# Performance work log

Hardware: AMD Instinct MI355X
Metric: run time of the kernel (lower is better)

The kernel has to match this reference:

```python
import jax, jax.numpy as jnp
import numpy as np

B, D_IN, H, A, L, HEADS, C = 1024, 512, 768, 5001, 4, 2, 2
N_DATA = 56000.0
NEG = -1e30


def _gru_step(x, h, Wih, Whh, bih, bhh):
    # torch nn.GRU gate order: r, z, n
    gi = x @ Wih + bih            # [B, 3H]
    gh = h @ Whh + bhh            # [B, 3H]
    i_r, i_z, i_n = jnp.split(gi, 3, axis=-1)
    h_r, h_z, h_n = jnp.split(gh, 3, axis=-1)
    r = jax.nn.sigmoid(i_r + h_r)
    z = jax.nn.sigmoid(i_z + h_z)
    n = jnp.tanh(i_n + r * h_n)
    return (1.0 - z) * n + z * h


def _atom_selector(cls, mask, Wih, Whh, bih, bhh, hW, hb, ae_w, key):
    # cls: [B, H]; mask: [B, A] int32 (mutable copy); dropout in eval mode (identity)
    h = jnp.zeros_like(cls)
    cur_in = cls
    ae_const = jax.lax.stop_gradient(ae_w)
    probs = []
    max_index = None
    rows = jnp.arange(B)
    for j in range(L):
        h = _gru_step(cur_in, h, Wih, Whh, bih, bhh)
        logits = h @ hW + hb                      # [B, A]
        if j == 0:
            col0 = jnp.where(mask.sum(axis=-1) == 0, 1, mask[:, 0])
            mask = mask.at[:, 0].set(col0)
        else:
            mask = jnp.where((max_index == 0)[:, None], 0, mask)
            mask = mask.at[:, 0].set(1)
        masked = jnp.where(mask > 0, logits, NEG)
        u = jax.random.uniform(jax.random.fold_in(key, j), (B, A), minval=1e-9, maxval=1.0)
        g = -jnp.log(-jnp.log(u))
        y_soft = jax.nn.softmax(masked + g, axis=-1)  # tau = 1
        ind = jnp.argmax(y_soft, axis=-1)             # [B]
        y_hard = jax.nn.one_hot(ind, A, dtype=y_soft.dtype)
        prob = y_hard + y_soft - jax.lax.stop_gradient(y_soft)  # straight-through
        mask = mask.at[rows, ind].set(0)              # scatter-zero chosen atoms
        probs.append(prob)
        max_index = ind
        cur_in = cls + prob @ ae_const                # atom embedding feedback
    return jnp.stack(probs, axis=1)                   # [B, L, A]


def reference(x, x_mask, W1, b1, W2, b2, W3, b3, gru_Wih, gru_Whh, gru_bih, gru_bhh,
              head_W, head_b, ae_w, ce_Wmu, ce_bmu, ce_Wcov, ce_bcov, alpha):
    # linear_base MLP
    h = jax.nn.relu(x @ W1 + b1)
    h = jax.nn.relu(h @ W2 + b2)
    h = h @ W3 + b3                                   # cls embedding [B, H]
    key = jax.random.key(42)
    atom_probs, cps = [], []
    for i in range(HEADS):
        ap = _atom_selector(h, x_mask, gru_Wih[i], gru_Whh[i], gru_bih[i], gru_bhh[i],
                            head_W[i], head_b[i], ae_w, jax.random.fold_in(key, i))
        atom_probs.append(ap)
        # consequent estimator stand-in: mu [B,C], coverage [B]
        pooled = ap.mean(axis=1)                      # [B, A]
        mu = jax.nn.sigmoid(pooled @ ce_Wmu + ce_bmu)
        coverage = jax.nn.sigmoid(pooled @ ce_Wcov + ce_bcov)
        n = coverage * N_DATA
        sf = (alpha[0] / n)[:, None]                  # [B, 1] -> broadcast to [B, C]
        cp = (mu + sf) / (1.0 + 2.0 * sf)
        cps.append(cp)
    mat_cp = jnp.stack(cps, axis=1)                   # [B, HEADS, C]
    out = jnp.log(mat_cp.mean(axis=1))                # [B, C]
    return out, jnp.stack(atom_probs, axis=1), mat_cp


def setup_inputs() -> dict:
    key = jax.random.key(0)
    ks = jax.random.split(key, 16)
    s = 0.02
    nrm = lambda k, sh: jax.random.normal(k, sh, dtype=jnp.float32) * s
    return {
        'x': jax.random.normal(ks[0], (B, D_IN), dtype=jnp.float32),
        'x_mask': jax.random.randint(ks[1], (B, A), 0, 2, dtype=jnp.int32),
        'W1': nrm(ks[2], (D_IN, H)), 'b1': jnp.zeros((H,), jnp.float32),
        'W2': nrm(ks[3], (H, H)), 'b2': jnp.zeros((H,), jnp.float32),
        'W3': nrm(ks[4], (H, H)), 'b3': jnp.zeros((H,), jnp.float32),
        'gru_Wih': nrm(ks[5], (HEADS, H, 3 * H)), 'gru_Whh': nrm(ks[6], (HEADS, H, 3 * H)),
        'gru_bih': jnp.zeros((HEADS, 3 * H), jnp.float32), 'gru_bhh': jnp.zeros((HEADS, 3 * H), jnp.float32),
        'head_W': nrm(ks[7], (HEADS, H, A)), 'head_b': jnp.zeros((HEADS, A), jnp.float32),
        'ae_w': nrm(ks[8], (A, H)),
        'ce_Wmu': nrm(ks[9], (A, C)), 'ce_bmu': jnp.zeros((C,), jnp.float32),
        'ce_Wcov': nrm(ks[10], (A,)), 'ce_bcov': jnp.zeros((), jnp.float32),
        'alpha': jnp.ones((1,), jnp.float32),
    }
```

## Files before the change

kernel.cpp:

```cpp
#include <hip/hip_runtime.h>
#include <hip/hip_bf16.h>
#include <stdint.h>
#include <stddef.h>

#define B_DIM   1024
#define DIN     512
#define H_DIM   768
#define A_DIM   5001
#define NHEADS  2
#define NSTEPS  4
#define C_DIM   2
#define NEG_VAL -1e30f
#define BH      (B_DIM * H_DIM)

typedef unsigned short u16;
typedef __attribute__((ext_vector_type(8))) short v8s;
typedef __attribute__((ext_vector_type(4))) float v4f;

typedef const __attribute__((address_space(1))) uint32_t* gas_ptr;
typedef __attribute__((address_space(3))) uint32_t* las_ptr;

__device__ __forceinline__ void load_lds16(const void* g, void* l) {
  __builtin_amdgcn_global_load_lds((gas_ptr)g, (las_ptr)l, 16, 0, 0);
}

__host__ __device__ inline uint32_t rotl32(uint32_t x, int d) {
  return (x << d) | (x >> (32 - d));
}

__host__ __device__ inline void threefry2x32(uint32_t k0, uint32_t k1,
                                             uint32_t x0, uint32_t x1,
                                             uint32_t& o0, uint32_t& o1) {
  uint32_t ks2 = k0 ^ k1 ^ 0x1BD11BDAu;
  x0 += k0; x1 += k1;
#define TFR(d) { x0 += x1; x1 = rotl32(x1, (d)); x1 ^= x0; }
  TFR(13) TFR(15) TFR(26) TFR(6)  x0 += k1;  x1 += ks2 + 1u;
  TFR(17) TFR(29) TFR(16) TFR(24) x0 += ks2; x1 += k0 + 2u;
  TFR(13) TFR(15) TFR(26) TFR(6)  x0 += k0;  x1 += k1 + 3u;
  TFR(17) TFR(29) TFR(16) TFR(24) x0 += k1;  x1 += ks2 + 4u;
  TFR(13) TFR(15) TFR(26) TFR(6)  x0 += ks2; x1 += k0 + 5u;
#undef TFR
  o0 = x0; o1 = x1;
}

__device__ inline float gumbel_noise(uint32_t k0, uint32_t k1, uint32_t idx) {
  uint32_t o0, o1;
  threefry2x32(k0, k1, 0u, idx, o0, o1);
  uint32_t bits = o0 ^ o1;
  float f = __uint_as_float(0x3f800000u | (bits >> 9)) - 1.0f;
  float u = fmaxf(1e-9f, f * (1.0f - 1e-9f) + 1e-9f);
  return -logf(-logf(u));
}

__device__ inline float sigmoidf_(float x) { return 0.5f * tanhf(0.5f * x) + 0.5f; }

__device__ inline void split_bf16(float x, u16& hi, u16& lo) {
  __hip_bfloat16 h = __float2bfloat16(x);
  float hf = __bfloat162float(h);
  __hip_bfloat16 l = __float2bfloat16(x - hf);
  hi = *(const u16*)&h;
  lo = *(const u16*)&l;
}

__global__ __launch_bounds__(256) void gemm_splitk(
    const float* __restrict__ A, const float* __restrict__ B,
    float* __restrict__ part, int M, int N, int K, int kchunk) {
  __shared__ float As[16][65];
  __shared__ float Bs[16][64];
  int tid = threadIdx.x;
  int bm = blockIdx.y * 64, bn = blockIdx.x * 64;
  const int s = blockIdx.z;
  const int kb = s * kchunk;
  const int ke = (kb + kchunk < K) ? (kb + kchunk) : K;
  int tx = tid & 15, ty = tid >> 4;
  float acc[4][4] = {};
  for (int k0 = kb; k0 < ke; k0 += 16) {
#pragma unroll
    for (int r = 0; r < 4; ++r) {
      int m = (tid >> 4) + r * 16;
      int k = tid & 15;
      As[k][m] = A[(size_t)(bm + m) * K + k0 + k];
    }
#pragma unroll
    for (int r = 0; r < 4; ++r) {
      int n = tid & 63;
      int k = (tid >> 6) + r * 4;
      int gn = bn + n;
      Bs[k][n] = (gn < N) ? B[(size_t)(k0 + k) * N + gn] : 0.0f;
    }
    __syncthreads();
#pragma unroll
    for (int kk = 0; kk < 16; ++kk) {
      float a[4], bb[4];
#pragma unroll
      for (int i = 0; i < 4; ++i) a[i] = As[kk][ty * 4 + i];
#pragma unroll
      for (int jj = 0; jj < 4; ++jj) bb[jj] = Bs[kk][tx * 4 + jj];
#pragma unroll
      for (int i = 0; i < 4; ++i)
#pragma unroll
        for (int jj = 0; jj < 4; ++jj) acc[i][jj] = fmaf(a[i], bb[jj], acc[i][jj]);
    }
    __syncthreads();
  }
  float* po = part + (size_t)s * M * N;
#pragma unroll
  for (int i = 0; i < 4; ++i) {
    int m = bm + ty * 4 + i;
#pragma unroll
    for (int jj = 0; jj < 4; ++jj) {
      int n = bn + tx * 4 + jj;
      if (n < N) po[(size_t)m * N + n] = acc[i][jj];
    }
  }
}

__global__ __launch_bounds__(256) void reduce_bias_act(
    const float* __restrict__ part, const float* __restrict__ bias,
    float* __restrict__ C, int M, int N, int S, int act) {
  int idx = blockIdx.x * blockDim.x + threadIdx.x;
  if (idx >= M * N) return;
  int n = idx % N;
  float v = 0.0f;
  for (int s = 0; s < S; ++s) v += part[(size_t)s * M * N + idx];
  v += bias[n];
  if (act == 1) v = fmaxf(v, 0.0f);
  C[idx] = v;
}

__global__ __launch_bounds__(256) void transpose_split(
    const float* __restrict__ W, u16* __restrict__ hi, u16* __restrict__ lo,
    int K, int N, size_t inStride, size_t outStride) {
  const int e = blockIdx.z;
  const float* Win = W + (size_t)e * inStride;
  u16* ho = hi + (size_t)e * outStride;
  u16* loo = lo + (size_t)e * outStride;
  __shared__ float tile[32][33];
  const int k0 = blockIdx.y * 32, n0 = blockIdx.x * 32;
  const int tx = threadIdx.x & 31, ty = threadIdx.x >> 5;
#pragma unroll
  for (int r = ty; r < 32; r += 8) {
    int n = n0 + tx;
    tile[r][tx] = (n < N) ? Win[(size_t)(k0 + r) * N + n] : 0.0f;
  }
  __syncthreads();
#pragma unroll
  for (int r = ty; r < 32; r += 8) {
    int n = n0 + r, k = k0 + tx;
    if (n < N) {
      u16 h, l;
      split_bf16(tile[tx][r], h, l);
      ho[(size_t)n * K + k] = h;
      loo[(size_t)n * K + k] = l;
    }
  }
}

struct GemmS {
  const u16* Ah[4]; const u16* Al[4];
  const u16* Bh[4]; const u16* Bl[4];
  const float* bias[4]; float* C[4];
};

__global__ __launch_bounds__(256, 2) void gemm_mfma(
    GemmS gs, int K, int N, int Nclamp, long long ldc, int nbx, int nby) {
  const int e = blockIdx.y;
  const int nwg = nbx * nby;
  const int chunk = nwg >> 3;
  const int orig = blockIdx.x;
  const int lid = (orig & 7) * chunk + (orig >> 3);
  const int by = lid % nby;
  const int bx = lid / nby;
  const int bm = by * 128, bn = bx * 128;

  __shared__ __align__(16) u16 lds[4][128 * 32];

  const int tid = threadIdx.x;
  const int wv = tid >> 6, ln = tid & 63;
  const int wr = wv >> 1, wc = wv & 1;
  const int lk = ln >> 4;
  const int lm = ln & 15;
  const int fswz = (lm >> 1) & 3;

  const int lrow = ln >> 2;
  const int slot = (ln & 3) ^ ((lrow >> 1) & 3);
  const u16* tsrc = (wv == 0) ? gs.Ah[e] : (wv == 1) ? gs.Al[e]
                  : (wv == 2) ? gs.Bh[e] : gs.Bl[e];
  const int isB = (wv >= 2);
  const int rowbase = isB ? bn : bm;

  const float* bias = gs.bias[e];
  float* C = gs.C[e];

  v4f acc[4][4];
#pragma unroll
  for (int i = 0; i < 4; ++i)
#pragma unroll
    for (int j = 0; j < 4; ++j) acc[i][j] = (v4f){0.f, 0.f, 0.f, 0.f};

  for (int k0 = 0; k0 < K; k0 += 32) {
#pragma unroll
    for (int i = 0; i < 8; ++i) {
      int gr = rowbase + i * 16 + lrow;
      if (isB && gr >= Nclamp) gr = Nclamp - 1;
      const u16* gp = tsrc + (size_t)gr * K + k0 + slot * 8;
      load_lds16(gp, (void*)&lds[wv][i * 512]);
    }
    __syncthreads();

    v8s ah[4], al[4], bh[4], bl[4];
#pragma unroll
    for (int mi = 0; mi < 4; ++mi) {
      const int r = wr * 64 + mi * 16 + lm;
      const int off = r * 32 + ((lk ^ fswz) * 8);
      ah[mi] = *(const v8s*)&lds[0][off];
      al[mi] = *(const v8s*)&lds[1][off];
    }
#pragma unroll
    for (int ni = 0; ni < 4; ++ni) {
      const int r = wc * 64 + ni * 16 + lm;
      const int off = r * 32 + ((lk ^ fswz) * 8);
      bh[ni] = *(const v8s*)&lds[2][off];
      bl[ni] = *(const v8s*)&lds[3][off];
    }
#pragma unroll
    for (int mi = 0; mi < 4; ++mi)
#pragma unroll
      for (int ni = 0; ni < 4; ++ni)
        acc[mi][ni] = __builtin_amdgcn_mfma_f32_16x16x32_bf16(ah[mi], bh[ni], acc[mi][ni], 0, 0, 0);
#pragma unroll
    for (int mi = 0; mi < 4; ++mi)
#pragma unroll
      for (int ni = 0; ni < 4; ++ni)
        acc[mi][ni] = __builtin_amdgcn_mfma_f32_16x16x32_bf16(ah[mi], bl[ni], acc[mi][ni], 0, 0, 0);
#pragma unroll
    for (int mi = 0; mi < 4; ++mi)
#pragma unroll
      for (int ni = 0; ni < 4; ++ni)
        acc[mi][ni] = __builtin_amdgcn_mfma_f32_16x16x32_bf16(al[mi], bh[ni], acc[mi][ni], 0, 0, 0);

    __syncthreads();
  }

#pragma unroll
  for (int mi = 0; mi < 4; ++mi) {
    const int m = bm + wr * 64 + mi * 16 + lk * 4;
#pragma unroll
    for (int ni = 0; ni < 4; ++ni) {
      const int n = bn + wc * 64 + ni * 16 + lm;
      if (n < N) {
        const float bv = bias[n];
        float* cp = C + (size_t)m * ldc + n;
#pragma unroll
        for (int r = 0; r < 4; ++r)
          cp[(size_t)r * ldc] = acc[mi][ni][r] + bv;
      }
    }
  }
}

__global__ __launch_bounds__(256) void init_state_kernel(
    const float* __restrict__ cls,
    u16* __restrict__ cur_hi, u16* __restrict__ cur_lo) {
  int idx = blockIdx.x * blockDim.x + threadIdx.x;
  if (idx >= 2 * BH) return;
  int rem = idx % BH;
  u16 h, l;
  split_bf16(cls[rem], h, l);
  cur_hi[idx] = h; cur_lo[idx] = l;
}

__global__ __launch_bounds__(256) void gru_combine_first(
    const float* __restrict__ gi2, const float* __restrict__ gbhh, float* __restrict__ h2,
    u16* __restrict__ h_hi, u16* __restrict__ h_lo) {
  int idx = blockIdx.x * blockDim.x + threadIdx.x;
  if (idx >= 2 * BH) return;
  int e = idx / BH, rem = idx % BH;
  int b = rem / H_DIM, c = rem - b * H_DIM;
  const float* gib = gi2 + ((size_t)e * B_DIM + b) * 3 * H_DIM;
  const float* bb = gbhh + (size_t)e * 3 * H_DIM;
  float ir = gib[c], iz = gib[H_DIM + c], inn = gib[2 * H_DIM + c];
  float hr = bb[c], hz = bb[H_DIM + c], hn = bb[2 * H_DIM + c];
  float r = sigmoidf_(ir + hr);
  float z = sigmoidf_(iz + hz);
  float n = tanhf(inn + r * hn);
  float hv = (1.0f - z) * n + z * 0.0f;
  h2[idx] = hv;
  u16 h, l;
  split_bf16(hv, h, l);
  h_hi[idx] = h; h_lo[idx] = l;
}

__global__ __launch_bounds__(256) void gru_combine_kernel(
    const float* __restrict__ gi2, const float* __restrict__ gh2, float* __restrict__ h2,
    u16* __restrict__ h_hi, u16* __restrict__ h_lo) {
  int idx = blockIdx.x * blockDim.x + threadIdx.x;
  if (idx >= 2 * BH) return;
  int e = idx / BH, rem = idx % BH;
  int b = rem / H_DIM, c = rem - b * H_DIM;
  const float* gib = gi2 + ((size_t)e * B_DIM + b) * 3 * H_DIM;
  const float* ghb = gh2 + ((size_t)e * B_DIM + b) * 3 * H_DIM;
  float ir = gib[c], iz = gib[H_DIM + c], inn = gib[2 * H_DIM + c];
  float hr = ghb[c], hz = ghb[H_DIM + c], hn = ghb[2 * H_DIM + c];
  float r = sigmoidf_(ir + hr);
  float z = sigmoidf_(iz + hz);
  float n = tanhf(inn + r * hn);
  float hv = (1.0f - z) * n + z * h2[idx];
  h2[idx] = hv;
  u16 h, l;
  split_bf16(hv, h, l);
  h_hi[idx] = h; h_lo[idx] = l;
}

__global__ __launch_bounds__(256) void curin_kernel(
    const float* __restrict__ cls, const float* __restrict__ ae_w,
    const int* __restrict__ indb, int j,
    u16* __restrict__ cur_hi, u16* __restrict__ cur_lo) {
  int idx = blockIdx.x * blockDim.x + threadIdx.x;
  if (idx >= 2 * BH) return;
  int e = idx / BH, rem = idx % BH;
  int b = rem / H_DIM, c = rem - b * H_DIM;
  int ind = indb[(e * NSTEPS + j) * B_DIM + b];
  float v = cls[rem] + ae_w[(size_t)ind * H_DIM + c];
  u16 h, l;
  split_bf16(v, h, l);
  cur_hi[idx] = h; cur_lo[idx] = l;
}

#define STH 256
#define PER_TH 20

__global__ __launch_bounds__(STH) void sample_kernel(
    float* __restrict__ probs, const int* __restrict__ x_mask,
    int* __restrict__ indb, int j, uint4 keys) {
  int b = blockIdx.x;
  int e = blockIdx.y;
  int t = threadIdx.x;
  uint32_t k0 = (e == 0) ? keys.x : keys.z;
  uint32_t k1 = (e == 0) ? keys.y : keys.w;
  __shared__ float rv[STH];
  __shared__ int ri[STH];
  __shared__ int s_ind;

  float* prow = probs + (((size_t)b * NHEADS + e) * NSTEPS + j) * A_DIM;
  const int* mrow = x_mask + (size_t)b * A_DIM;

  int prev[3];
  bool dead = false;
  for (int tt = 0; tt < j; ++tt) {
    prev[tt] = indb[(e * NSTEPS + tt) * B_DIM + b];
    if (prev[tt] == 0) dead = true;
  }

  bool rowany = true;
  if (j == 0) {
    int any = 0;
    for (int a = t; a < A_DIM; a += STH) any |= mrow[a];
    ri[t] = any; __syncthreads();
    for (int s = STH / 2; s > 0; s >>= 1) {
      if (t < s) ri[t] |= ri[t + s];
      __syncthreads();
    }
    rowany = (ri[0] != 0);
    __syncthreads();
  }

  float v[PER_TH];
  float lmax = -3.0e38f;
#pragma unroll
  for (int s = 0; s < PER_TH; ++s) {
    int a = t + s * STH;
    float val = -3.0e38f;
    if (a < A_DIM) {
      int m;
      if (j == 0) {
        m = (a == 0) ? (rowany ? mrow[0] : 1) : mrow[a];
      } else if (a == 0) {
        m = 1;
      } else if (dead) {
        m = 0;
      } else {
        m = mrow[a];
        if (m) {
          for (int tt = 0; tt < j; ++tt)
            if (prev[tt] == a) { m = 0; break; }
        }
      }
      if (m > 0)
        val = prow[a] + gumbel_noise(k0, k1, (uint32_t)(b * A_DIM + a));
    }
    v[s] = val;
    lmax = fmaxf(lmax, val);
  }

  rv[t] = lmax; __syncthreads();
  for (int s = STH / 2; s > 0; s >>= 1) {
    if (t < s) rv[t] = fmaxf(rv[t], rv[t + s]);
    __syncthreads();
  }
  float m = rv[0]; __syncthreads();

  float lsum = 0.0f;
#pragma unroll
  for (int s = 0; s < PER_TH; ++s) {
    int a = t + s * STH;
    float ev = (a < A_DIM && v[s] > -1.0e37f) ? expf(v[s] - m) : 0.0f;
    v[s] = ev; lsum += ev;
  }
  rv[t] = lsum; __syncthreads();
  for (int s = STH / 2; s > 0; s >>= 1) {
    if (t < s) rv[t] += rv[t + s];
    __syncthreads();
  }
  float ssum = rv[0]; __syncthreads();

  float besty = -1.0f; int besti = A_DIM;
#pragma unroll
  for (int s = 0; s < PER_TH; ++s) {
    int a = t + s * STH;
    if (a < A_DIM) {
      float y = v[s] / ssum;
      if (y > besty) { besty = y; besti = a; }
    }
  }
  rv[t] = besty; ri[t] = besti; __syncthreads();
  for (int s = STH / 2; s > 0; s >>= 1) {
    if (t < s) {
      float y2 = rv[t + s]; int i2 = ri[t + s];
      if (y2 > rv[t] || (y2 == rv[t] && i2 < ri[t])) { rv[t] = y2; ri[t] = i2; }
    }
    __syncthreads();
  }
  if (t == 0) { s_ind = ri[0]; indb[(e * NSTEPS + j) * B_DIM + b] = ri[0]; }
  __syncthreads();
  int ind = s_ind;

  for (int a = t; a < A_DIM; a += STH) prow[a] = (a == ind) ? 1.0f : 0.0f;
}

__global__ __launch_bounds__(256) void head_final_kernel(
    const int* __restrict__ indb, const float* __restrict__ Wmu,
    const float* __restrict__ bmu, const float* __restrict__ Wcov,
    const float* __restrict__ bcov, const float* __restrict__ alpha,
    float* __restrict__ matcp) {
  int idx = blockIdx.x * blockDim.x + threadIdx.x;
  if (idx >= NHEADS * B_DIM) return;
  int e = idx / B_DIM, b = idx - e * B_DIM;
  float a0 = 0.0f, a1 = 0.0f, ac = 0.0f;
  for (int j = 0; j < NSTEPS; ++j) {
    int ind = indb[(e * NSTEPS + j) * B_DIM + b];
    a0 += 0.25f * Wmu[(size_t)ind * C_DIM + 0];
    a1 += 0.25f * Wmu[(size_t)ind * C_DIM + 1];
    ac += 0.25f * Wcov[ind];
  }
  float mu0 = sigmoidf_(a0 + bmu[0]);
  float mu1 = sigmoidf_(a1 + bmu[1]);
  float cov = sigmoidf_(ac + bcov[0]);
  float n = cov * 56000.0f;
  float sf = alpha[0] / n;
  float denom = 1.0f + 2.0f * sf;
  matcp[((size_t)b * NHEADS + e) * C_DIM + 0] = (mu0 + sf) / denom;
  matcp[((size_t)b * NHEADS + e) * C_DIM + 1] = (mu1 + sf) / denom;
}

__global__ __launch_bounds__(256) void final_out_kernel(
    const float* __restrict__ matcp, float* __restrict__ out) {
  int idx = blockIdx.x * blockDim.x + threadIdx.x;
  if (idx >= B_DIM * C_DIM) return;
  int b = idx / C_DIM, c = idx - b * C_DIM;
  float s = matcp[((size_t)b * NHEADS + 0) * C_DIM + c] +
            matcp[((size_t)b * NHEADS + 1) * C_DIM + c];
  out[idx] = logf(s * 0.5f);
}

extern "C" void kernel_launch(void* const* d_in, const int* in_sizes, int n_in,
                              void* d_out, int out_size, void* d_ws, size_t ws_size,
                              hipStream_t stream) {
  const float* x     = (const float*)d_in[0];
  const int*   xmask = (const int*)d_in[1];
  const float* W1 = (const float*)d_in[2];  const float* b1 = (const float*)d_in[3];
  const float* W2 = (const float*)d_in[4];  const float* b2 = (const float*)d_in[5];
  const float* W3 = (const float*)d_in[6];  const float* b3 = (const float*)d_in[7];
  const float* gWih = (const float*)d_in[8];  const float* gWhh = (const float*)d_in[9];
  const float* gbih = (const float*)d_in[10]; const float* gbhh = (const float*)d_in[11];
  const float* hW = (const float*)d_in[12];   const float* hb = (const float*)d_in[13];
  const float* ae_w = (const float*)d_in[14];
  const float* Wmu  = (const float*)d_in[15]; const float* bmu  = (const float*)d_in[16];
  const float* Wcov = (const float*)d_in[17]; const float* bcov = (const float*)d_in[18];
  const float* alpha = (const float*)d_in[19];

  float* out = (float*)d_out;
  float* probs = out + (size_t)B_DIM * C_DIM;
  float* matcp = probs + (size_t)B_DIM * NHEADS * NSTEPS * A_DIM;

  const int HG = 3 * H_DIM;
  uint8_t* wsp = (uint8_t*)d_ws;
  auto alloc = [&](size_t bytes) {
    uint8_t* p = wsp;
    wsp += (bytes + 255) & ~(size_t)255;
    return p;
  };
  float* cls  = (float*)alloc((size_t)BH * 4);
  float* h2   = (float*)alloc((size_t)2 * BH * 4);
  float* gi2  = (float*)alloc((size_t)2 * B_DIM * HG * 4);
  float* gh2  = (float*)alloc((size_t)2 * B_DIM * HG * 4);
  u16* h_hi   = (u16*)alloc((size_t)2 * BH * 2);
  u16* h_lo   = (u16*)alloc((size_t)2 * BH * 2);
  u16* cur_hi = (u16*)alloc((size_t)2 * BH * 2);
  u16* cur_lo = (u16*)alloc((size_t)2 * BH * 2);
  u16* WihT_h = (u16*)alloc((size_t)2 * HG * H_DIM * 2);
  u16* WihT_l = (u16*)alloc((size_t)2 * HG * H_DIM * 2);
  u16* WhhT_h = (u16*)alloc((size_t)2 * HG * H_DIM * 2);
  u16* WhhT_l = (u16*)alloc((size_t)2 * HG * H_DIM * 2);
  u16* hWT_h  = (u16*)alloc((size_t)2 * A_DIM * H_DIM * 2);
  u16* hWT_l  = (u16*)alloc((size_t)2 * A_DIM * H_DIM * 2);
  int* indb   = (int*)alloc((size_t)NHEADS * NSTEPS * B_DIM * 4);
  float* parts = gh2;
  float* t1 = gi2;
  float* t2 = gi2 + BH;

  dim3 blk(256);

  transpose_split<<<dim3(HG / 32, H_DIM / 32, 2), blk, 0, stream>>>(
      gWih, WihT_h, WihT_l, H_DIM, HG, (size_t)H_DIM * HG, (size_t)HG * H_DIM);
  transpose_split<<<dim3(HG / 32, H_DIM / 32, 2), blk, 0, stream>>>(
      gWhh, WhhT_h, WhhT_l, H_DIM, HG, (size_t)H_DIM * HG, (size_t)HG * H_DIM);
  transpose_split<<<dim3((A_DIM + 31) / 32, H_DIM / 32, 2), blk, 0, stream>>>(
      hW, hWT_h, hWT_l, H_DIM, A_DIM, (size_t)H_DIM * A_DIM, (size_t)A_DIM * H_DIM);

  const int MN = B_DIM * H_DIM;
  gemm_splitk<<<dim3(H_DIM / 64, B_DIM / 64, 4), blk, 0, stream>>>(
      x, W1, parts, B_DIM, H_DIM, DIN, 128);
  reduce_bias_act<<<(MN + 255) / 256, blk, 0, stream>>>(parts, b1, t1, B_DIM, H_DIM, 4, 1);
  gemm_splitk<<<dim3(H_DIM / 64, B_DIM / 64, 6), blk, 0, stream>>>(
      t1, W2, parts, B_DIM, H_DIM, H_DIM, 128);
  reduce_bias_act<<<(MN + 255) / 256, blk, 0, stream>>>(parts, b2, t2, B_DIM, H_DIM, 6, 1);
  gemm_splitk<<<dim3(H_DIM / 64, B_DIM / 64, 6), blk, 0, stream>>>(
      t2, W3, parts, B_DIM, H_DIM, H_DIM, 128);
  reduce_bias_act<<<(MN + 255) / 256, blk, 0, stream>>>(parts, b3, cls, B_DIM, H_DIM, 6, 0);

  init_state_kernel<<<(2 * BH + 255) / 256, blk, 0, stream>>>(cls, cur_hi, cur_lo);

  uint32_t bk0 = 0u, bk1 = 42u;
  uint32_t hk[2][2];
  threefry2x32(bk0, bk1, 0u, 0u, hk[0][0], hk[0][1]);
  threefry2x32(bk0, bk1, 0u, 1u, hk[1][0], hk[1][1]);

  for (int j = 0; j < NSTEPS; ++j) {
    if (j == 0) {
      GemmS gb;
      for (int head = 0; head < NHEADS; ++head) {
        gb.Ah[head] = cur_hi + (size_t)head * BH;
        gb.Al[head] = cur_lo + (size_t)head * BH;
        gb.Bh[head] = WihT_h + (size_t)head * HG * H_DIM;
        gb.Bl[head] = WihT_l + (size_t)head * HG * H_DIM;
        gb.bias[head] = gbih + (size_t)head * HG;
        gb.C[head] = gi2 + (size_t)head * B_DIM * HG;
        gb.Ah[head + 2] = gb.Ah[head]; gb.Al[head + 2] = gb.Al[head];
        gb.Bh[head + 2] = gb.Bh[head]; gb.Bl[head + 2] = gb.Bl[head];
        gb.bias[head + 2] = gb.bias[head]; gb.C[head + 2] = gb.C[head];
      }
      gemm_mfma<<<dim3((HG / 128) * (B_DIM / 128), 2), blk, 0, stream>>>(
          gb, H_DIM, HG, HG, (long long)HG, HG / 128, B_DIM / 128);
      gru_combine_first<<<(2 * BH + 255) / 256, blk, 0, stream>>>(gi2, gbhh, h2, h_hi, h_lo);
    } else {
      GemmS gb;
      for (int head = 0; head < NHEADS; ++head) {
        gb.Ah[head * 2 + 0] = cur_hi + (size_t)head * BH;
        gb.Al[head * 2 + 0] = cur_lo + (size_t)head * BH;
        gb.Bh[head * 2 + 0] = WihT_h + (size_t)head * HG * H_DIM;
        gb.Bl[head * 2 + 0] = WihT_l + (size_t)head * HG * H_DIM;
        gb.bias[head * 2 + 0] = gbih + (size_t)head * HG;
        gb.C[head * 2 + 0] = gi2 + (size_t)head * B_DIM * HG;
        gb.Ah[head * 2 + 1] = h_hi + (size_t)head * BH;
        gb.Al[head * 2 + 1] = h_lo + (size_t)head * BH;
        gb.Bh[head * 2 + 1] = WhhT_h + (size_t)head * HG * H_DIM;
        gb.Bl[head * 2 + 1] = WhhT_l + (size_t)head * HG * H_DIM;
        gb.bias[head * 2 + 1] = gbhh + (size_t)head * HG;
        gb.C[head * 2 + 1] = gh2 + (size_t)head * B_DIM * HG;
      }
      gemm_mfma<<<dim3((HG / 128) * (B_DIM / 128), 4), blk, 0, stream>>>(
          gb, H_DIM, HG, HG, (long long)HG, HG / 128, B_DIM / 128);
      gru_combine_kernel<<<(2 * BH + 255) / 256, blk, 0, stream>>>(gi2, gh2, h2, h_hi, h_lo);
    }

    GemmS lb;
    for (int head = 0; head < NHEADS; ++head) {
      lb.Ah[head] = h_hi + (size_t)head * BH;
      lb.Al[head] = h_lo + (size_t)head * BH;
      lb.Bh[head] = hWT_h + (size_t)head * A_DIM * H_DIM;
      lb.Bl[head] = hWT_l + (size_t)head * A_DIM * H_DIM;
      lb.bias[head] = hb + (size_t)head * A_DIM;
      lb.C[head] = probs + (size_t)(head * NSTEPS + j) * A_DIM;
      lb.Ah[head + 2] = lb.Ah[head]; lb.Al[head + 2] = lb.Al[head];
      lb.Bh[head + 2] = lb.Bh[head]; lb.Bl[head + 2] = lb.Bl[head];
      lb.bias[head + 2] = lb.bias[head]; lb.C[head + 2] = lb.C[head];
    }
    gemm_mfma<<<dim3(40 * (B_DIM / 128), 2), blk, 0, stream>>>(
        lb, H_DIM, A_DIM, A_DIM, (long long)NHEADS * NSTEPS * A_DIM, 40, B_DIM / 128);

    uint32_t s00, s01, s10, s11;
    threefry2x32(hk[0][0], hk[0][1], 0u, (uint32_t)j, s00, s01);
    threefry2x32(hk[1][0], hk[1][1], 0u, (uint32_t)j, s10, s11);
    uint4 keys; keys.x = s00; keys.y = s01; keys.z = s10; keys.w = s11;
    sample_kernel<<<dim3(B_DIM, NHEADS), dim3(STH), 0, stream>>>(probs, xmask, indb, j, keys);

    if (j < NSTEPS - 1)
      curin_kernel<<<(2 * BH + 255) / 256, blk, 0, stream>>>(cls, ae_w, indb, j, cur_hi, cur_lo);
  }

  head_final_kernel<<<(NHEADS * B_DIM + 255) / 256, blk, 0, stream>>>(
      indb, Wmu, bmu, Wcov, bcov, alpha, matcp);
  final_out_kernel<<<(B_DIM * C_DIM + 255) / 256, blk, 0, stream>>>(matcp, out);
}
```

Measured before the change: 832.7 us.

## Run base MLP on split-bf16 MFMA GEMM and fuse cur_in into sampler

```diff
diff --git a/kernel.cpp b/kernel.cpp
--- a/kernel.cpp
+++ b/kernel.cpp
@@ -62,70 +62,13 @@
   lo = *(const u16*)&l;
 }
 
-__global__ __launch_bounds__(256) void gemm_splitk(
-    const float* __restrict__ A, const float* __restrict__ B,
-    float* __restrict__ part, int M, int N, int K, int kchunk) {
-  __shared__ float As[16][65];
-  __shared__ float Bs[16][64];
-  int tid = threadIdx.x;
-  int bm = blockIdx.y * 64, bn = blockIdx.x * 64;
-  const int s = blockIdx.z;
-  const int kb = s * kchunk;
-  const int ke = (kb + kchunk < K) ? (kb + kchunk) : K;
-  int tx = tid & 15, ty = tid >> 4;
-  float acc[4][4] = {};
-  for (int k0 = kb; k0 < ke; k0 += 16) {
-#pragma unroll
-    for (int r = 0; r < 4; ++r) {
-      int m = (tid >> 4) + r * 16;
-      int k = tid & 15;
-      As[k][m] = A[(size_t)(bm + m) * K + k0 + k];
-    }
-#pragma unroll
-    for (int r = 0; r < 4; ++r) {
-      int n = tid & 63;
-      int k = (tid >> 6) + r * 4;
-      int gn = bn + n;
-      Bs[k][n] = (gn < N) ? B[(size_t)(k0 + k) * N + gn] : 0.0f;
-    }
-    __syncthreads();
-#pragma unroll
-    for (int kk = 0; kk < 16; ++kk) {
-      float a[4], bb[4];
-#pragma unroll
-      for (int i = 0; i < 4; ++i) a[i] = As[kk][ty * 4 + i];
-#pragma unroll
-      for (int jj = 0; jj < 4; ++jj) bb[jj] = Bs[kk][tx * 4 + jj];
-#pragma unroll
-      for (int i = 0; i < 4; ++i)
-#pragma unroll
-        for (int jj = 0; jj < 4; ++jj) acc[i][jj] = fmaf(a[i], bb[jj], acc[i][jj]);
-    }
-    __syncthreads();
-  }
-  float* po = part + (size_t)s * M * N;
-#pragma unroll
-  for (int i = 0; i < 4; ++i) {
-    int m = bm + ty * 4 + i;
-#pragma unroll
-    for (int jj = 0; jj < 4; ++jj) {
-      int n = bn + tx * 4 + jj;
-      if (n < N) po[(size_t)m * N + n] = acc[i][jj];
-    }
-  }
-}
-
-__global__ __launch_bounds__(256) void reduce_bias_act(
-    const float* __restrict__ part, const float* __restrict__ bias,
-    float* __restrict__ C, int M, int N, int S, int act) {
+__global__ __launch_bounds__(256) void split_kernel(
+    const float* __restrict__ in, u16* __restrict__ hi, u16* __restrict__ lo, int n) {
   int idx = blockIdx.x * blockDim.x + threadIdx.x;
-  if (idx >= M * N) return;
-  int n = idx % N;
-  float v = 0.0f;
-  for (int s = 0; s < S; ++s) v += part[(size_t)s * M * N + idx];
-  v += bias[n];
-  if (act == 1) v = fmaxf(v, 0.0f);
-  C[idx] = v;
+  if (idx >= n) return;
+  u16 h, l;
+  split_bf16(in[idx], h, l);
+  hi[idx] = h; lo[idx] = l;
 }
 
 __global__ __launch_bounds__(256) void transpose_split(
@@ -160,10 +103,11 @@
   const u16* Ah[4]; const u16* Al[4];
   const u16* Bh[4]; const u16* Bl[4];
   const float* bias[4]; float* C[4];
+  u16* Ch[4]; u16* Cl[4];
 };
 
 __global__ __launch_bounds__(256, 2) void gemm_mfma(
-    GemmS gs, int K, int N, int Nclamp, long long ldc, int nbx, int nby) {
+    GemmS gs, int K, int N, int Nclamp, long long ldc, int nbx, int nby, int act) {
   const int e = blockIdx.y;
   const int nwg = nbx * nby;
   const int chunk = nwg >> 3;
@@ -190,7 +134,6 @@
   const int rowbase = isB ? bn : bm;
 
   const float* bias = gs.bias[e];
-  float* C = gs.C[e];
 
   v4f acc[4][4];
 #pragma unroll
@@ -242,18 +185,46 @@
     __syncthreads();
   }
 
-#pragma unroll
-  for (int mi = 0; mi < 4; ++mi) {
-    const int m = bm + wr * 64 + mi * 16 + lk * 4;
-#pragma unroll
-    for (int ni = 0; ni < 4; ++ni) {
-      const int n = bn + wc * 64 + ni * 16 + lm;
-      if (n < N) {
-        const float bv = bias[n];
-        float* cp = C + (size_t)m * ldc + n;
-#pragma unroll
-        for (int r = 0; r < 4; ++r)
-          cp[(size_t)r * ldc] = acc[mi][ni][r] + bv;
+  if (gs.Ch[e]) {
+    u16* ch = gs.Ch[e]; u16* cl = gs.Cl[e];
+#pragma unroll
+    for (int mi = 0; mi < 4; ++mi) {
+      const int m = bm + wr * 64 + mi * 16 + lk * 4;
+#pragma unroll
+      for (int ni = 0; ni < 4; ++ni) {
+        const int n = bn + wc * 64 + ni * 16 + lm;
+        if (n < N) {
+          const float bv = bias[n];
+#pragma unroll
+          for (int r = 0; r < 4; ++r) {
+            float v = acc[mi][ni][r] + bv;
+            if (act) v = fmaxf(v, 0.0f);
+            u16 hh, ll;
+            split_bf16(v, hh, ll);
+            ch[(size_t)(m + r) * ldc + n] = hh;
+            cl[(size_t)(m + r) * ldc + n] = ll;
+          }
+        }
+      }
+    }
+  } else {
+    float* C = gs.C[e];
+#pragma unroll
+    for (int mi = 0; mi < 4; ++mi) {
+      const int m = bm + wr * 64 + mi * 16 + lk * 4;
+#pragma unroll
+      for (int ni = 0; ni < 4; ++ni) {
+        const int n = bn + wc * 64 + ni * 16 + lm;
+        if (n < N) {
+          const float bv = bias[n];
+          float* cp = C + (size_t)m * ldc + n;
+#pragma unroll
+          for (int r = 0; r < 4; ++r) {
+            float v = acc[mi][ni][r] + bv;
+            if (act) v = fmaxf(v, 0.0f);
+            cp[(size_t)r * ldc] = v;
+          }
+        }
       }
     }
   }
@@ -312,27 +283,14 @@
   h_hi[idx] = h; h_lo[idx] = l;
 }
 
-__global__ __launch_bounds__(256) void curin_kernel(
-    const float* __restrict__ cls, const float* __restrict__ ae_w,
-    const int* __restrict__ indb, int j,
-    u16* __restrict__ cur_hi, u16* __restrict__ cur_lo) {
-  int idx = blockIdx.x * blockDim.x + threadIdx.x;
-  if (idx >= 2 * BH) return;
-  int e = idx / BH, rem = idx % BH;
-  int b = rem / H_DIM, c = rem - b * H_DIM;
-  int ind = indb[(e * NSTEPS + j) * B_DIM + b];
-  float v = cls[rem] + ae_w[(size_t)ind * H_DIM + c];
-  u16 h, l;
-  split_bf16(v, h, l);
-  cur_hi[idx] = h; cur_lo[idx] = l;
-}
-
 #define STH 256
 #define PER_TH 20
 
 __global__ __launch_bounds__(STH) void sample_kernel(
     float* __restrict__ probs, const int* __restrict__ x_mask,
-    int* __restrict__ indb, int j, uint4 keys) {
+    int* __restrict__ indb, int j, uint4 keys,
+    const float* __restrict__ cls, const float* __restrict__ ae_w,
+    u16* __restrict__ cur_hi, u16* __restrict__ cur_lo, int docur) {
   int b = blockIdx.x;
   int e = blockIdx.y;
   int t = threadIdx.x;
@@ -436,6 +394,19 @@
   int ind = s_ind;
 
   for (int a = t; a < A_DIM; a += STH) prow[a] = (a == ind) ? 1.0f : 0.0f;
+
+  if (docur) {
+    const float* crow = cls + (size_t)b * H_DIM;
+    const float* arow = ae_w + (size_t)ind * H_DIM;
+    u16* chh = cur_hi + (size_t)e * BH + (size_t)b * H_DIM;
+    u16* cll = cur_lo + (size_t)e * BH + (size_t)b * H_DIM;
+    for (int c = t; c < H_DIM; c += STH) {
+      float vv = crow[c] + arow[c];
+      u16 hh, ll;
+      split_bf16(vv, hh, ll);
+      chh[c] = hh; cll[c] = ll;
+    }
+  }
 }
 
 __global__ __launch_bounds__(256) void head_final_kernel(
@@ -514,10 +485,19 @@
   u16* WhhT_l = (u16*)alloc((size_t)2 * HG * H_DIM * 2);
   u16* hWT_h  = (u16*)alloc((size_t)2 * A_DIM * H_DIM * 2);
   u16* hWT_l  = (u16*)alloc((size_t)2 * A_DIM * H_DIM * 2);
+  u16* x_hi   = (u16*)alloc((size_t)B_DIM * DIN * 2);
+  u16* x_lo   = (u16*)alloc((size_t)B_DIM * DIN * 2);
+  u16* t1_hi  = (u16*)alloc((size_t)BH * 2);
+  u16* t1_lo  = (u16*)alloc((size_t)BH * 2);
+  u16* t2_hi  = (u16*)alloc((size_t)BH * 2);
+  u16* t2_lo  = (u16*)alloc((size_t)BH * 2);
+  u16* W1T_h  = (u16*)alloc((size_t)H_DIM * DIN * 2);
+  u16* W1T_l  = (u16*)alloc((size_t)H_DIM * DIN * 2);
+  u16* W2T_h  = (u16*)alloc((size_t)H_DIM * H_DIM * 2);
+  u16* W2T_l  = (u16*)alloc((size_t)H_DIM * H_DIM * 2);
+  u16* W3T_h  = (u16*)alloc((size_t)H_DIM * H_DIM * 2);
+  u16* W3T_l  = (u16*)alloc((size_t)H_DIM * H_DIM * 2);
   int* indb   = (int*)alloc((size_t)NHEADS * NSTEPS * B_DIM * 4);
-  float* parts = gh2;
-  float* t1 = gi2;
-  float* t2 = gi2 + BH;
 
   dim3 blk(256);
 
@@ -527,17 +507,35 @@
       gWhh, WhhT_h, WhhT_l, H_DIM, HG, (size_t)H_DIM * HG, (size_t)HG * H_DIM);
   transpose_split<<<dim3((A_DIM + 31) / 32, H_DIM / 32, 2), blk, 0, stream>>>(
       hW, hWT_h, hWT_l, H_DIM, A_DIM, (size_t)H_DIM * A_DIM, (size_t)A_DIM * H_DIM);
-
-  const int MN = B_DIM * H_DIM;
-  gemm_splitk<<<dim3(H_DIM / 64, B_DIM / 64, 4), blk, 0, stream>>>(
-      x, W1, parts, B_DIM, H_DIM, DIN, 128);
-  reduce_bias_act<<<(MN + 255) / 256, blk, 0, stream>>>(parts, b1, t1, B_DIM, H_DIM, 4, 1);
-  gemm_splitk<<<dim3(H_DIM / 64, B_DIM / 64, 6), blk, 0, stream>>>(
-      t1, W2, parts, B_DIM, H_DIM, H_DIM, 128);
-  reduce_bias_act<<<(MN + 255) / 256, blk, 0, stream>>>(parts, b2, t2, B_DIM, H_DIM, 6, 1);
-  gemm_splitk<<<dim3(H_DIM / 64, B_DIM / 64, 6), blk, 0, stream>>>(
-      t2, W3, parts, B_DIM, H_DIM, H_DIM, 128);
-  reduce_bias_act<<<(MN + 255) / 256, blk, 0, stream>>>(parts, b3, cls, B_DIM, H_DIM, 6, 0);
+  transpose_split<<<dim3(H_DIM / 32, DIN / 32, 1), blk, 0, stream>>>(
+      W1, W1T_h, W1T_l, DIN, H_DIM, 0, 0);
+  transpose_split<<<dim3(H_DIM / 32, H_DIM / 32, 1), blk, 0, stream>>>(
+      W2, W2T_h, W2T_l, H_DIM, H_DIM, 0, 0);
+  transpose_split<<<dim3(H_DIM / 32, H_DIM / 32, 1), blk, 0, stream>>>(
+      W3, W3T_h, W3T_l, H_DIM, H_DIM, 0, 0);
+  split_kernel<<<(B_DIM * DIN + 255) / 256, blk, 0, stream>>>(x, x_hi, x_lo, B_DIM * DIN);
+
+  {
+    GemmS g{};
+    g.Ah[0] = x_hi; g.Al[0] = x_lo; g.Bh[0] = W1T_h; g.Bl[0] = W1T_l;
+    g.bias[0] = b1; g.C[0] = nullptr; g.Ch[0] = t1_hi; g.Cl[0] = t1_lo;
+    gemm_mfma<<<dim3((H_DIM / 128) * (B_DIM / 128), 1), blk, 0, stream>>>(
+        g, DIN, H_DIM, H_DIM, (long long)H_DIM, H_DIM / 128, B_DIM / 128, 1);
+  }
+  {
+    GemmS g{};
+    g.Ah[0] = t1_hi; g.Al[0] = t1_lo; g.Bh[0] = W2T_h; g.Bl[0] = W2T_l;
+    g.bias[0] = b2; g.C[0] = nullptr; g.Ch[0] = t2_hi; g.Cl[0] = t2_lo;
+    gemm_mfma<<<dim3((H_DIM / 128) * (B_DIM / 128), 1), blk, 0, stream>>>(
+        g, H_DIM, H_DIM, H_DIM, (long long)H_DIM, H_DIM / 128, B_DIM / 128, 1);
+  }
+  {
+    GemmS g{};
+    g.Ah[0] = t2_hi; g.Al[0] = t2_lo; g.Bh[0] = W3T_h; g.Bl[0] = W3T_l;
+    g.bias[0] = b3; g.C[0] = cls; g.Ch[0] = nullptr;
+    gemm_mfma<<<dim3((H_DIM / 128) * (B_DIM / 128), 1), blk, 0, stream>>>(
+        g, H_DIM, H_DIM, H_DIM, (long long)H_DIM, H_DIM / 128, B_DIM / 128, 0);
+  }
 
   init_state_kernel<<<(2 * BH + 255) / 256, blk, 0, stream>>>(cls, cur_hi, cur_lo);
 
@@ -548,7 +546,7 @@
 
   for (int j = 0; j < NSTEPS; ++j) {
     if (j == 0) {
-      GemmS gb;
+      GemmS gb{};
       for (int head = 0; head < NHEADS; ++head) {
         gb.Ah[head] = cur_hi + (size_t)head * BH;
         gb.Al[head] = cur_lo + (size_t)head * BH;
@@ -556,15 +554,12 @@
         gb.Bl[head] = WihT_l + (size_t)head * HG * H_DIM;
         gb.bias[head] = gbih + (size_t)head * HG;
         gb.C[head] = gi2 + (size_t)head * B_DIM * HG;
-        gb.Ah[head + 2] = gb.Ah[head]; gb.Al[head + 2] = gb.Al[head];
-        gb.Bh[head + 2] = gb.Bh[head]; gb.Bl[head + 2] = gb.Bl[head];
-        gb.bias[head + 2] = gb.bias[head]; gb.C[head + 2] = gb.C[head];
       }
       gemm_mfma<<<dim3((HG / 128) * (B_DIM / 128), 2), blk, 0, stream>>>(
-          gb, H_DIM, HG, HG, (long long)HG, HG / 128, B_DIM / 128);
+          gb, H_DIM, HG, HG, (long long)HG, HG / 128, B_DIM / 128, 0);
       gru_combine_first<<<(2 * BH + 255) / 256, blk, 0, stream>>>(gi2, gbhh, h2, h_hi, h_lo);
     } else {
-      GemmS gb;
+      GemmS gb{};
       for (int head = 0; head < NHEADS; ++head) {
         gb.Ah[head * 2 + 0] = cur_hi + (size_t)head * BH;
         gb.Al[head * 2 + 0] = cur_lo + (size_t)head * BH;
@@ -580,11 +575,11 @@
         gb.C[head * 2 + 1] = gh2 + (size_t)head * B_DIM * HG;
       }
       gemm_mfma<<<dim3((HG / 128) * (B_DIM / 128), 4), blk, 0, stream>>>(
-          gb, H_DIM, HG, HG, (long long)HG, HG / 128, B_DIM / 128);
+          gb, H_DIM, HG, HG, (long long)HG, HG / 128, B_DIM / 128, 0);
       gru_combine_kernel<<<(2 * BH + 255) / 256, blk, 0, stream>>>(gi2, gh2, h2, h_hi, h_lo);
     }
 
-    GemmS lb;
+    GemmS lb{};
     for (int head = 0; head < NHEADS; ++head) {
       lb.Ah[head] = h_hi + (size_t)head * BH;
       lb.Al[head] = h_lo + (size_t)head * BH;
@@ -592,21 +587,16 @@
       lb.Bl[head] = hWT_l + (size_t)head * A_DIM * H_DIM;
       lb.bias[head] = hb + (size_t)head * A_DIM;
       lb.C[head] = probs + (size_t)(head * NSTEPS + j) * A_DIM;
-      lb.Ah[head + 2] = lb.Ah[head]; lb.Al[head + 2] = lb.Al[head];
-      lb.Bh[head + 2] = lb.Bh[head]; lb.Bl[head + 2] = lb.Bl[head];
-      lb.bias[head + 2] = lb.bias[head]; lb.C[head + 2] = lb.C[head];
     }
     gemm_mfma<<<dim3(40 * (B_DIM / 128), 2), blk, 0, stream>>>(
-        lb, H_DIM, A_DIM, A_DIM, (long long)NHEADS * NSTEPS * A_DIM, 40, B_DIM / 128);
+        lb, H_DIM, A_DIM, A_DIM, (long long)NHEADS * NSTEPS * A_DIM, 40, B_DIM / 128, 0);
 
     uint32_t s00, s01, s10, s11;
     threefry2x32(hk[0][0], hk[0][1], 0u, (uint32_t)j, s00, s01);
     threefry2x32(hk[1][0], hk[1][1], 0u, (uint32_t)j, s10, s11);
     uint4 keys; keys.x = s00; keys.y = s01; keys.z = s10; keys.w = s11;
-    sample_kernel<<<dim3(B_DIM, NHEADS), dim3(STH), 0, stream>>>(probs, xmask, indb, j, keys);
-
-    if (j < NSTEPS - 1)
-      curin_kernel<<<(2 * BH + 255) / 256, blk, 0, stream>>>(cls, ae_w, indb, j, cur_hi, cur_lo);
+    sample_kernel<<<dim3(B_DIM, NHEADS), dim3(STH), 0, stream>>>(
+        probs, xmask, indb, j, keys, cls, ae_w, cur_hi, cur_lo, (j < NSTEPS - 1) ? 1 : 0);
   }
 
   head_final_kernel<<<(NHEADS * B_DIM + 255) / 256, blk, 0, stream>>>(
```

Result: no change. 838.7 us (+0.7%).
